# Optimization experiments

Hardware: AMD Instinct MI355X
Metric: run time of the kernel (lower is better)

The kernel has to match this reference:

```python
import jax, jax.numpy as jnp
import numpy as np

NEG_SLOPE = 0.2  # PyG GATConv default leaky_relu slope
N_NODES, N_EDGES, F_IN, HID = 25000, 200000, 64, 128


def gat_layer(x, src, dst, W, a_src, a_dst, b, heads, ch):
    """PyG-style GATConv (concat=True, eval mode). x:[N,Fin] -> [N,heads*ch]."""
    N = x.shape[0]
    h = (x @ W).reshape(N, heads, ch)                      # [N,H,C]
    al_s = jnp.sum(h * a_src, axis=-1)                     # [N,H]
    al_d = jnp.sum(h * a_dst, axis=-1)                     # [N,H]
    e = jax.nn.leaky_relu(al_s[src] + al_d[dst], NEG_SLOPE)  # [E,H]
    # segment softmax over incoming edges of each dst node (stable)
    e = e - jax.ops.segment_max(e, dst, num_segments=N)[dst]
    ex = jnp.exp(e)
    alpha = ex / jax.ops.segment_sum(ex, dst, num_segments=N)[dst]  # [E,H]
    out = jax.ops.segment_sum(h[src] * alpha[:, :, None], dst, num_segments=N)  # [N,H,C]
    return out.reshape(N, heads * ch) + b


def setup_inputs() -> dict:
    key = jax.random.key(0)
    ks = jax.random.split(key, 24)
    def g(k, shape, fan_in):
        return jax.random.normal(k, shape, dtype=jnp.float32) / np.sqrt(fan_in)
    inp = {
        "x": jax.random.normal(ks[0], (N_NODES, F_IN), dtype=jnp.float32),
        "edge_index": jax.random.randint(ks[1], (2, N_EDGES), 0, N_NODES, dtype=jnp.int64) if jax.config.jax_enable_x64 else jax.random.randint(ks[1], (2, N_EDGES), 0, N_NODES).astype(jnp.int32),
        "liquor_idx": jax.random.randint(ks[2], (4096,), 0, N_NODES),
        "ingredient_idx": jax.random.randint(ks[3], (4096,), 0, N_NODES),
        "W1": g(ks[4], (F_IN, 8 * HID), F_IN), "a_s1": g(ks[5], (8, HID), HID), "a_d1": g(ks[6], (8, HID), HID), "b1": jnp.zeros((8 * HID,), jnp.float32),
        "W2": g(ks[7], (8 * HID, 8 * HID), 8 * HID), "a_s2": g(ks[8], (8, HID), HID), "a_d2": g(ks[9], (8, HID), HID), "b2": jnp.zeros((8 * HID,), jnp.float32),
        "W3": g(ks[10], (8 * HID, HID), 8 * HID), "a_s3": g(ks[11], (1, HID), HID), "a_d3": g(ks[12], (1, HID), HID), "b3": jnp.zeros((HID,), jnp.float32),
        # MLP scorer: 256 -> 128 -> 64 -> 1
        "mw1": g(ks[13], (2 * HID, HID), 2 * HID), "mb1": jnp.zeros((HID,), jnp.float32),
        "mw2": g(ks[14], (HID, HID // 2), HID), "mb2": jnp.zeros((HID // 2,), jnp.float32),
        "mw3": g(ks[15], (HID // 2, 1), HID // 2), "mb3": jnp.zeros((1,), jnp.float32),
    }
    return inp


def reference(x, edge_index, liquor_idx, ingredient_idx,
              W1, a_s1, a_d1, b1, W2, a_s2, a_d2, b2, W3, a_s3, a_d3, b3,
              mw1, mb1, mw2, mb2, mw3, mb3):
    N = x.shape[0]
    loops = jnp.arange(N, dtype=edge_index.dtype)  # GATConv adds self-loops
    src = jnp.concatenate([edge_index[0], loops])
    dst = jnp.concatenate([edge_index[1], loops])
    h = jax.nn.relu(gat_layer(x, src, dst, W1, a_s1, a_d1, b1, 8, HID))
    h = jax.nn.relu(gat_layer(h, src, dst, W2, a_s2, a_d2, b2, 8, HID))
    h = gat_layer(h, src, dst, W3, a_s3, a_d3, b3, 1, HID)
    pair = jnp.concatenate([h[liquor_idx], h[ingredient_idx]], axis=-1)  # [B,256]
    z = jax.nn.relu(pair @ mw1 + mb1)
    z = jax.nn.relu(z @ mw2 + mb2)
    z = z @ mw3 + mb3
    return jax.nn.sigmoid(z).squeeze(-1)
```

## Files before the change

kernel.cpp:

```cpp
#include <hip/hip_runtime.h>
#include <math.h>

#define NEG_SLOPE 0.2f

typedef short short8 __attribute__((ext_vector_type(8)));
typedef float f32x4 __attribute__((ext_vector_type(4)));

__device__ __forceinline__ float lrelu(float x){ return x > 0.f ? x : NEG_SLOPE * x; }

__device__ __forceinline__ unsigned short f2bf(float f){
  union { float f; unsigned u; } v; v.f = f;
  unsigned r = v.u + 0x7fff + ((v.u >> 16) & 1);
  return (unsigned short)(r >> 16);
}
__device__ __forceinline__ float bf2f(unsigned short u){
  union { unsigned u; float f; } v; v.u = ((unsigned)u) << 16; return v.f;
}

__device__ __forceinline__ void gld16(const unsigned short* g, unsigned short* l){
  __builtin_amdgcn_global_load_lds(
      (const __attribute__((address_space(1))) unsigned int*)g,
      (__attribute__((address_space(3))) unsigned int*)l, 16, 0, 0);
}

__global__ void k_count(const int* __restrict__ dst, int* __restrict__ cnt, int E){
  int e = blockIdx.x*blockDim.x + threadIdx.x;
  if (e < E) atomicAdd(&cnt[dst[e]], 1);
}

__global__ void k_blockscan(const int* __restrict__ cnt, int* __restrict__ row,
                            int* __restrict__ aux, int n){
  __shared__ int buf[256];
  int t = threadIdx.x;
  int base = blockIdx.x * 256;
  int v = (base + t < n) ? cnt[base + t] : 0;
  buf[t] = v;
  __syncthreads();
  #pragma unroll
  for (int off = 1; off < 256; off <<= 1){
    int u = (t >= off) ? buf[t - off] : 0;
    __syncthreads();
    buf[t] += u;
    __syncthreads();
  }
  if (base + t < n) row[base + t + 1] = buf[t];
  if (t == 255) aux[blockIdx.x] = buf[255];
  if (blockIdx.x == 0 && t == 0) row[0] = 0;
}

__global__ void k_addoff(const int* __restrict__ aux, int* __restrict__ row, int n){
  __shared__ int s_pre;
  int b = blockIdx.x, t = threadIdx.x;
  if (t == 0){
    int pre = 0;
    for (int i = 0; i < b; ++i) pre += aux[i];
    s_pre = pre;
  }
  __syncthreads();
  int i = b * 256 + t;
  if (i < n) row[i + 1] += s_pre;
}

__global__ void k_scatter(const int* __restrict__ src, const int* __restrict__ dst,
                          const int* __restrict__ row, int* __restrict__ cur,
                          int* __restrict__ csr, int E){
  int e = blockIdx.x*blockDim.x + threadIdx.x;
  if (e < E){
    int d = dst[e];
    int p = atomicAdd(&cur[d], 1);
    csr[row[d] + p] = src[e];
  }
}

__global__ void k_prep(const float* __restrict__ x, unsigned short* __restrict__ xb, int nx, int nxb,
                       const float* __restrict__ W1, unsigned short* __restrict__ Wt1,
                       const float* __restrict__ W2, unsigned short* __restrict__ Wt2,
                       const float* __restrict__ W3, unsigned short* __restrict__ Wt3){
  __shared__ float tile[32][33];
  int b = blockIdx.x, t = threadIdx.x;
  if (b < nxb){
    int i0 = b * 2048 + t * 8;
    if (i0 + 8 <= nx){
      float4 f0 = *reinterpret_cast<const float4*>(x + i0);
      float4 f1 = *reinterpret_cast<const float4*>(x + i0 + 4);
      short8 o;
      o[0]=f2bf(f0.x); o[1]=f2bf(f0.y); o[2]=f2bf(f0.z); o[3]=f2bf(f0.w);
      o[4]=f2bf(f1.x); o[5]=f2bf(f1.y); o[6]=f2bf(f1.z); o[7]=f2bf(f1.w);
      *reinterpret_cast<short8*>(xb + i0) = o;
    } else {
      for (int k = 0; k < 8 && i0 + k < nx; ++k) xb[i0 + k] = f2bf(x[i0 + k]);
    }
    return;
  }
  const float* W; unsigned short* Wt; int K, N, ti;
  if (b < nxb + 64)            { W = W1; Wt = Wt1; K = 64;   N = 1024; ti = b - nxb;
                                 int kb = (ti & 1) * 32, nb = (ti >> 1) * 32;
                                 int tx = t & 31, ty = t >> 5;
                                 #pragma unroll
                                 for (int i = ty; i < 32; i += 8) tile[i][tx] = W[(size_t)(kb+i)*N + nb+tx];
                                 __syncthreads();
                                 #pragma unroll
                                 for (int i = ty; i < 32; i += 8) Wt[(size_t)(nb+i)*K + kb+tx] = f2bf(tile[tx][i]);
                                 return; }
  if (b < nxb + 64 + 1024)     { W = W2; Wt = Wt2; K = 1024; N = 1024; ti = b - nxb - 64; }
  else                         { W = W3; Wt = Wt3; K = 1024; N = 128;  ti = b - nxb - 64 - 1024; }
  int kb = (ti & 31) * 32, nb = (ti >> 5) * 32;
  int tx = t & 31, ty = t >> 5;
  #pragma unroll
  for (int i = ty; i < 32; i += 8) tile[i][tx] = W[(size_t)(kb+i)*N + nb+tx];
  __syncthreads();
  #pragma unroll
  for (int i = ty; i < 32; i += 8) Wt[(size_t)(nb+i)*K + kb+tx] = f2bf(tile[tx][i]);
}

template<int HEADS>
__global__ __launch_bounds__(256) void k_gemm_fused(
    const unsigned short* __restrict__ A,
    const unsigned short* __restrict__ Bt,
    unsigned short* __restrict__ C,
    const float* __restrict__ a_s, const float* __restrict__ a_d,
    float* __restrict__ ALS, float* __restrict__ ALD,
    int M, int N, int K, int gxc){
  __shared__ unsigned short SMEM[2 * 128 * 32];
  unsigned short* As = SMEM;
  unsigned short* Bs = SMEM + 128 * 32;
  const int nwg = gridDim.x;
  int bid = blockIdx.x;
  int swz = ((nwg & 7) == 0) ? ((bid & 7) * (nwg >> 3) + (bid >> 3)) : bid;
  const int bxi = swz % gxc, byi = swz / gxc;
  const int bm = byi * 128, bn = bxi * 128;
  const int head = bxi;
  const int tid  = threadIdx.x;
  const int lane = tid & 63, wave = tid >> 6;
  const int wr = wave >> 1, wc = wave & 1;
  const int lr = lane & 15, lk = lane >> 4;
  const int srow = wave * 16 + (lane >> 2);
  const int skc  = (lane & 3) * 8;
  int ar0 = bm + srow;      if (ar0 >= M) ar0 = M - 1;
  int ar1 = bm + srow + 64; if (ar1 >= M) ar1 = M - 1;
  const unsigned short* ga0 = A  + (size_t)ar0 * K + skc;
  const unsigned short* ga1 = A  + (size_t)ar1 * K + skc;
  const unsigned short* gb0 = Bt + (size_t)(bn + srow) * K + skc;
  const unsigned short* gb1 = Bt + (size_t)(bn + srow + 64) * K + skc;
  f32x4 acc[4][4] = {};
  for (int k0 = 0; k0 < K; k0 += 32){
    gld16(ga0 + k0, &As[(size_t)wave * 512]);
    gld16(ga1 + k0, &As[(size_t)(wave + 4) * 512]);
    gld16(gb0 + k0, &Bs[(size_t)wave * 512]);
    gld16(gb1 + k0, &Bs[(size_t)(wave + 4) * 512]);
    __syncthreads();
    short8 af[4], bg[4];
    #pragma unroll
    for (int m = 0; m < 4; ++m)
      af[m] = *reinterpret_cast<const short8*>(&As[(wr * 64 + m * 16 + lr) * 32 + lk * 8]);
    #pragma unroll
    for (int n = 0; n < 4; ++n)
      bg[n] = *reinterpret_cast<const short8*>(&Bs[(wc * 64 + n * 16 + lr) * 32 + lk * 8]);
    #pragma unroll
    for (int m = 0; m < 4; ++m)
      #pragma unroll
      for (int n = 0; n < 4; ++n)
        acc[m][n] = __builtin_amdgcn_mfma_f32_16x16x32_bf16(af[m], bg[n], acc[m][n], 0, 0, 0);
    __syncthreads();
  }
  #pragma unroll
  for (int m = 0; m < 4; ++m){
    #pragma unroll
    for (int j = 0; j < 4; ++j){
      int rowi = bm + wr * 64 + m * 16 + lk * 4 + j;
      if (rowi < M){
        #pragma unroll
        for (int n = 0; n < 4; ++n)
          C[(size_t)rowi * N + bn + wc * 64 + n * 16 + lr] = f2bf(acc[m][n][j]);
      }
    }
  }
  float as4[4], ad4[4];
  #pragma unroll
  for (int n = 0; n < 4; ++n){
    as4[n] = a_s[head * 128 + wc * 64 + n * 16 + lr];
    ad4[n] = a_d[head * 128 + wc * 64 + n * 16 + lr];
  }
  float* red = (float*)SMEM;
  #pragma unroll
  for (int m = 0; m < 4; ++m){
    #pragma unroll
    for (int j = 0; j < 4; ++j){
      float ps = 0.f;
      #pragma unroll
      for (int n = 0; n < 4; ++n) ps = fmaf(acc[m][n][j], as4[n], ps);
      red[(wr * 64 + m * 16 + lk * 4 + j) * 32 + wc * 16 + lr] = ps;
    }
  }
  __syncthreads();
  if (tid < 128){
    float s = 0.f;
    #pragma unroll
    for (int i = 0; i < 32; ++i) s += red[tid * 32 + ((i + tid) & 31)];
    int gr = bm + tid;
    if (gr < M) ALS[(size_t)gr * HEADS + head] = s;
  }
  __syncthreads();
  #pragma unroll
  for (int m = 0; m < 4; ++m){
    #pragma unroll
    for (int j = 0; j < 4; ++j){
      float pd = 0.f;
      #pragma unroll
      for (int n = 0; n < 4; ++n) pd = fmaf(acc[m][n][j], ad4[n], pd);
      red[(wr * 64 + m * 16 + lk * 4 + j) * 32 + wc * 16 + lr] = pd;
    }
  }
  __syncthreads();
  if (tid < 128){
    float s = 0.f;
    #pragma unroll
    for (int i = 0; i < 32; ++i) s += red[tid * 32 + ((i + tid) & 31)];
    int gr = bm + tid;
    if (gr < M) ALD[(size_t)gr * HEADS + head] = s;
  }
}

template<int HEADS, int VEC, int OUTBF>
__global__ void k_gat_bf(const unsigned short* __restrict__ hp, const float* __restrict__ al_s,
                         const float* __restrict__ al_d, const int* __restrict__ row,
                         const int* __restrict__ csr, const float* __restrict__ bias,
                         void* __restrict__ outv, int N, int do_relu){
  constexpr int TPH = 128 / VEC;
  int n = blockIdx.x;
  int t = threadIdx.x;
  int h = t / TPH;
  int c0 = (t % TPH) * VEC;
  float ald = al_d[(size_t)n * HEADS + h];
  float mA = lrelu(al_s[(size_t)n * HEADS + h] + ald);
  float lA = 1.f;
  float accA[VEC], accB[VEC];
  float mB = -1e30f, lB = 0.f;
  const unsigned short* hpn = hp + ((size_t)n * HEADS + h) * 128 + c0;
  if constexpr (VEC == 8){
    short8 hv8 = *reinterpret_cast<const short8*>(hpn);
    #pragma unroll
    for (int v = 0; v < 8; ++v){ accA[v] = bf2f((unsigned short)hv8[v]); accB[v] = 0.f; }
  } else {
    ushort2 hv2 = *reinterpret_cast<const ushort2*>(hpn);
    accA[0] = bf2f(hv2.x); accA[1] = bf2f(hv2.y);
    accB[0] = 0.f; accB[1] = 0.f;
  }
  int beg = row[n], end = row[n + 1];
  int j = beg;
  for (; j + 1 < end; j += 2){
    int s0 = csr[j], s1 = csr[j + 1];
    float e0 = lrelu(al_s[(size_t)s0 * HEADS + h] + ald);
    float e1 = lrelu(al_s[(size_t)s1 * HEADS + h] + ald);
    const unsigned short* p0 = hp + ((size_t)s0 * HEADS + h) * 128 + c0;
    const unsigned short* p1 = hp + ((size_t)s1 * HEADS + h) * 128 + c0;
    if constexpr (VEC == 8){
      short8 v0 = *reinterpret_cast<const short8*>(p0);
      short8 v1 = *reinterpret_cast<const short8*>(p1);
      float mn0 = fmaxf(mA, e0), mn1 = fmaxf(mB, e1);
      float sc0 = __expf(mA - mn0), sc1 = __expf(mB - mn1);
      float pw0 = __expf(e0 - mn0), pw1 = __expf(e1 - mn1);
      #pragma unroll
      for (int v = 0; v < 8; ++v){
        accA[v] = accA[v] * sc0 + pw0 * bf2f((unsigned short)v0[v]);
        accB[v] = accB[v] * sc1 + pw1 * bf2f((unsigned short)v1[v]);
      }
      lA = lA * sc0 + pw0; mA = mn0;
      lB = lB * sc1 + pw1; mB = mn1;
    } else {
      ushort2 v0 = *reinterpret_cast<const ushort2*>(p0);
      ushort2 v1 = *reinterpret_cast<const ushort2*>(p1);
      float mn0 = fmaxf(mA, e0), mn1 = fmaxf(mB, e1);
      float sc0 = __expf(mA - mn0), sc1 = __expf(mB - mn1);
      float pw0 = __expf(e0 - mn0), pw1 = __expf(e1 - mn1);
      accA[0] = accA[0] * sc0 + pw0 * bf2f(v0.x);
      accA[1] = accA[1] * sc0 + pw0 * bf2f(v0.y);
      accB[0] = accB[0] * sc1 + pw1 * bf2f(v1.x);
      accB[1] = accB[1] * sc1 + pw1 * bf2f(v1.y);
      lA = lA * sc0 + pw0; mA = mn0;
      lB = lB * sc1 + pw1; mB = mn1;
    }
  }
  if (j < end){
    int s0 = csr[j];
    float e0 = lrelu(al_s[(size_t)s0 * HEADS + h] + ald);
    const unsigned short* p0 = hp + ((size_t)s0 * HEADS + h) * 128 + c0;
    float mn0 = fmaxf(mA, e0);
    float sc0 = __expf(mA - mn0), pw0 = __expf(e0 - mn0);
    if constexpr (VEC == 8){
      short8 v0 = *reinterpret_cast<const short8*>(p0);
      #pragma unroll
      for (int v = 0; v < 8; ++v) accA[v] = accA[v] * sc0 + pw0 * bf2f((unsigned short)v0[v]);
    } else {
      ushort2 v0 = *reinterpret_cast<const ushort2*>(p0);
      accA[0] = accA[0] * sc0 + pw0 * bf2f(v0.x);
      accA[1] = accA[1] * sc0 + pw0 * bf2f(v0.y);
    }
    lA = lA * sc0 + pw0; mA = mn0;
  }
  float mn = fmaxf(mA, mB);
  float sA = __expf(mA - mn), sB = __expf(mB - mn);
  float l = lA * sA + lB * sB;
  float inv = 1.f / l;
  size_t ob = ((size_t)n * HEADS + h) * 128 + c0;
  #pragma unroll
  for (int v = 0; v < VEC; ++v){
    float o = (accA[v] * sA + accB[v] * sB) * inv + bias[h * 128 + c0 + v];
    if (do_relu) o = fmaxf(o, 0.f);
    if constexpr (OUTBF) ((unsigned short*)outv)[ob + v] = f2bf(o);
    else                 ((float*)outv)[ob + v] = o;
  }
}

__global__ void k_mlp(const float* __restrict__ h3, const int* __restrict__ liq,
                      const int* __restrict__ ing,
                      const float* __restrict__ mw1, const float* __restrict__ mb1,
                      const float* __restrict__ mw2, const float* __restrict__ mb2,
                      const float* __restrict__ mw3, const float* __restrict__ mb3,
                      float* __restrict__ out, int B){
  __shared__ float pairv[256];
  __shared__ float z1[128];
  __shared__ float z2[64];
  int r = blockIdx.x;
  int t = threadIdx.x;
  pairv[t]       = h3[(size_t)liq[r] * 128 + t];
  pairv[128 + t] = h3[(size_t)ing[r] * 128 + t];
  __syncthreads();
  float a1 = mb1[t];
  for (int k = 0; k < 256; ++k) a1 = fmaf(pairv[k], mw1[k * 128 + t], a1);
  z1[t] = fmaxf(a1, 0.f);
  __syncthreads();
  if (t < 64){
    float a2 = mb2[t];
    for (int k = 0; k < 128; ++k) a2 = fmaf(z1[k], mw2[k * 64 + t], a2);
    z2[t] = fmaxf(a2, 0.f);
  }
  __syncthreads();
  if (t < 64){
    float p = z2[t] * mw3[t];
    #pragma unroll
    for (int off = 32; off >= 1; off >>= 1) p += __shfl_xor(p, off);
    if (t == 0) out[r] = 1.f / (1.f + __expf(-(p + mb3[0])));
  }
}

extern "C" void kernel_launch(void* const* d_in, const int* in_sizes, int n_in,
                              void* d_out, int out_size, void* d_ws, size_t ws_size,
                              hipStream_t stream){
  const float* x   = (const float*)d_in[0];
  const int*   ei  = (const int*)  d_in[1];
  const int*   liq = (const int*)  d_in[2];
  const int*   ing = (const int*)  d_in[3];
  const float* W1  = (const float*)d_in[4];
  const float* as1 = (const float*)d_in[5];
  const float* ad1 = (const float*)d_in[6];
  const float* b1  = (const float*)d_in[7];
  const float* W2  = (const float*)d_in[8];
  const float* as2 = (const float*)d_in[9];
  const float* ad2 = (const float*)d_in[10];
  const float* b2  = (const float*)d_in[11];
  const float* W3  = (const float*)d_in[12];
  const float* as3 = (const float*)d_in[13];
  const float* ad3 = (const float*)d_in[14];
  const float* b3  = (const float*)d_in[15];
  const float* mw1 = (const float*)d_in[16];
  const float* mb1 = (const float*)d_in[17];
  const float* mw2 = (const float*)d_in[18];
  const float* mb2 = (const float*)d_in[19];
  const float* mw3 = (const float*)d_in[20];
  const float* mb3 = (const float*)d_in[21];
  float* out = (float*)d_out;

  const int N = in_sizes[0] / 64;
  const int E = in_sizes[1] / 2;
  const int B = in_sizes[2];
  const int* srcp = ei;
  const int* dstp = ei + E;

  char* w = (char*)d_ws;
  auto alloc = [&](size_t bytes) -> char* {
    char* p = w;
    w += (bytes + 255) & ~(size_t)255;
    return p;
  };
  unsigned short* P    = (unsigned short*)alloc((size_t)N * 1024 * 2);
  unsigned short* Hb   = (unsigned short*)alloc((size_t)N * 1024 * 2);
  float*          H3   = (float*)         alloc((size_t)N * 128 * 4);
  unsigned short* xb   = (unsigned short*)alloc((size_t)N * 64 * 2);
  unsigned short* Wt1  = (unsigned short*)alloc((size_t)1024 * 64 * 2);
  unsigned short* Wt2  = (unsigned short*)alloc((size_t)1024 * 1024 * 2);
  unsigned short* Wt3  = (unsigned short*)alloc((size_t)128 * 1024 * 2);
  float* ALS  = (float*)alloc((size_t)N * 8 * 4);
  float* ALD  = (float*)alloc((size_t)N * 8 * 4);
  int*   row  = (int*)  alloc((size_t)(N + 1) * 4);
  int*   cntcur = (int*)alloc((size_t)2 * N * 4);
  int*   cnt  = cntcur;
  int*   cur  = cntcur + N;
  int*   aux  = (int*)  alloc((size_t)256 * 4);
  int*   csr  = (int*)  alloc((size_t)E * 4);
  (void)ws_size; (void)n_in; (void)out_size;

  int nx = N * 64;
  int nxb = (nx + 2047) / 2048;
  k_prep<<<nxb + 64 + 1024 + 128, 256, 0, stream>>>(x, xb, nx, nxb, W1, Wt1, W2, Wt2, W3, Wt3);

  hipMemsetAsync(cntcur, 0, (size_t)2 * N * 4, stream);
  int eb = (E + 255) / 256;
  int nb = (N + 255) / 256;
  k_count<<<eb, 256, 0, stream>>>(dstp, cnt, E);
  k_blockscan<<<nb, 256, 0, stream>>>(cnt, row, aux, N);
  k_addoff<<<nb, 256, 0, stream>>>(aux, row, N);
  k_scatter<<<eb, 256, 0, stream>>>(srcp, dstp, row, cur, csr, E);

  const int mt = (N + 127) / 128;

  k_gemm_fused<8><<<8 * mt, 256, 0, stream>>>(xb, Wt1, P, as1, ad1, ALS, ALD, N, 1024, 64, 8);
  k_gat_bf<8,8,1><<<N, 128, 0, stream>>>(P, ALS, ALD, row, csr, b1, Hb, N, 1);

  k_gemm_fused<8><<<8 * mt, 256, 0, stream>>>(Hb, Wt2, P, as2, ad2, ALS, ALD, N, 1024, 1024, 8);
  k_gat_bf<8,8,1><<<N, 128, 0, stream>>>(P, ALS, ALD, row, csr, b2, Hb, N, 1);

  k_gemm_fused<1><<<1 * mt, 256, 0, stream>>>(Hb, Wt3, P, as3, ad3, ALS, ALD, N, 128, 1024, 1);
  k_gat_bf<1,2,0><<<N, 64, 0, stream>>>(P, ALS, ALD, row, csr, b3, H3, N, 0);

  k_mlp<<<B, 128, 0, stream>>>(H3, liq, ing, mw1, mb1, mw2, mb2, mw3, mb3, out, B);
}
```

Before: 363.3 us.

## Add 256x128-tile 8-wave GEMM with split-phase prefetch for layer-2 projection

Adds a new bf16 MFMA GEMM kernel for the 1024x1024 layer-2 projection. It uses 256-row tiles with 512 threads, double-buffered LDS filled by direct global-to-LDS loads, and B and A prefetches staggered across two MFMA phases with priority hints. It also computes both attention dot products (src and dst) in one shared-memory reduction pass. The larger tile is meant to raise operand reuse and overlap memory with compute. The cost is roughly 96KB of LDS per block and tight register use under launch_bounds(512,2), which can limit occupancy.

Result: no change. 356.7 us (-1.8%).

```diff
diff --git a/kernel.cpp b/kernel.cpp
--- a/kernel.cpp
+++ b/kernel.cpp
@@ -221,6 +221,160 @@
   }
 }
 
+__global__ __launch_bounds__(512, 2) void k_gemm256(
+    const unsigned short* __restrict__ A,
+    const unsigned short* __restrict__ Bt,
+    unsigned short* __restrict__ C,
+    const float* __restrict__ a_s, const float* __restrict__ a_d,
+    float* __restrict__ ALS, float* __restrict__ ALD,
+    int M, int N, int K, int gxc){
+  __shared__ unsigned short smem[2 * 24576];
+  const int nwg = gridDim.x;
+  int bid = blockIdx.x;
+  int swz = ((nwg & 7) == 0) ? ((bid & 7) * (nwg >> 3) + (bid >> 3)) : bid;
+  const int bxi = swz % gxc, byi = swz / gxc;
+  const int bm = byi * 256, bn = bxi * 128, head = bxi;
+  const int tid = threadIdx.x;
+  const int lane = tid & 63, wave = tid >> 6;
+  const int wr = wave >> 1, wc = wave & 1;
+  const int lr = lane & 15, lk = lane >> 4;
+  const int sr   = tid >> 3;
+  const int scol = ((tid & 7) << 3) ^ ((sr & 7) << 3);
+  size_t offA[4], offB[2];
+  #pragma unroll
+  for (int u = 0; u < 4; ++u){
+    int r = bm + u * 64 + sr; if (r >= M) r = M - 1;
+    offA[u] = (size_t)r * K + scol;
+  }
+  #pragma unroll
+  for (int u = 0; u < 2; ++u)
+    offB[u] = (size_t)(bn + u * 64 + sr) * K + scol;
+  const int wdst = (tid >> 6) * 512;
+
+  f32x4 acc[4][4] = {};
+  short8 af[4][2], bg[4][2];
+  const int NKT = K >> 6;
+  const int rsw = (lr & 7) << 3;
+
+  #pragma unroll
+  for (int u = 0; u < 4; ++u) gld16(A + offA[u], &smem[u * 4096 + wdst]);
+  #pragma unroll
+  for (int u = 0; u < 2; ++u) gld16(Bt + offB[u], &smem[16384 + u * 4096 + wdst]);
+  #pragma unroll
+  for (int u = 0; u < 4; ++u) gld16(A + offA[u] + 64, &smem[24576 + u * 4096 + wdst]);
+  asm volatile("s_waitcnt vmcnt(4)" ::: "memory");
+  __builtin_amdgcn_s_barrier();
+
+  for (int kt = 0; kt < NKT; ++kt){
+    const int s = kt & 1;
+    const unsigned short* sa = &smem[s * 24576];
+    const unsigned short* sb = &smem[s * 24576 + 16384];
+    #pragma unroll
+    for (int m = 0; m < 4; ++m){
+      int r = (wr * 64 + m * 16 + lr) * 64;
+      af[m][0] = *reinterpret_cast<const short8*>(&sa[r + ((lk * 8) ^ rsw)]);
+      af[m][1] = *reinterpret_cast<const short8*>(&sa[r + ((32 + lk * 8) ^ rsw)]);
+    }
+    #pragma unroll
+    for (int n = 0; n < 2; ++n){
+      int r = (wc * 64 + n * 16 + lr) * 64;
+      bg[n][0] = *reinterpret_cast<const short8*>(&sb[r + ((lk * 8) ^ rsw)]);
+      bg[n][1] = *reinterpret_cast<const short8*>(&sb[r + ((32 + lk * 8) ^ rsw)]);
+    }
+    if (kt + 1 < NKT){
+      int so = (s ^ 1) * 24576 + 16384;
+      gld16(Bt + offB[0] + (size_t)(kt + 1) * 64, &smem[so + wdst]);
+      gld16(Bt + offB[1] + (size_t)(kt + 1) * 64, &smem[so + 4096 + wdst]);
+    }
+    __builtin_amdgcn_s_barrier();
+    asm volatile("s_waitcnt lgkmcnt(0)" ::: "memory");
+    __builtin_amdgcn_sched_barrier(0);
+    __builtin_amdgcn_s_setprio(1);
+    #pragma unroll
+    for (int m = 0; m < 4; ++m)
+      #pragma unroll
+      for (int n = 0; n < 2; ++n){
+        acc[m][n] = __builtin_amdgcn_mfma_f32_16x16x32_bf16(af[m][0], bg[n][0], acc[m][n], 0, 0, 0);
+        acc[m][n] = __builtin_amdgcn_mfma_f32_16x16x32_bf16(af[m][1], bg[n][1], acc[m][n], 0, 0, 0);
+      }
+    __builtin_amdgcn_s_setprio(0);
+    __builtin_amdgcn_s_barrier();
+    #pragma unroll
+    for (int n = 2; n < 4; ++n){
+      int r = (wc * 64 + n * 16 + lr) * 64;
+      bg[n][0] = *reinterpret_cast<const short8*>(&sb[r + ((lk * 8) ^ rsw)]);
+      bg[n][1] = *reinterpret_cast<const short8*>(&sb[r + ((32 + lk * 8) ^ rsw)]);
+    }
+    if (kt + 2 < NKT){
+      int so = s * 24576;
+      #pragma unroll
+      for (int u = 0; u < 4; ++u)
+        gld16(A + offA[u] + (size_t)(kt + 2) * 64, &smem[so + u * 4096 + wdst]);
+    }
+    __builtin_amdgcn_s_barrier();
+    asm volatile("s_waitcnt lgkmcnt(0)" ::: "memory");
+    __builtin_amdgcn_sched_barrier(0);
+    __builtin_amdgcn_s_setprio(1);
+    #pragma unroll
+    for (int m = 0; m < 4; ++m)
+      #pragma unroll
+      for (int n = 2; n < 4; ++n){
+        acc[m][n] = __builtin_amdgcn_mfma_f32_16x16x32_bf16(af[m][0], bg[n][0], acc[m][n], 0, 0, 0);
+        acc[m][n] = __builtin_amdgcn_mfma_f32_16x16x32_bf16(af[m][1], bg[n][1], acc[m][n], 0, 0, 0);
+      }
+    __builtin_amdgcn_s_setprio(0);
+    asm volatile("s_waitcnt vmcnt(4)" ::: "memory");
+    __builtin_amdgcn_s_barrier();
+  }
+
+  #pragma unroll
+  for (int m = 0; m < 4; ++m)
+    #pragma unroll
+    for (int j = 0; j < 4; ++j){
+      int row = bm + wr * 64 + m * 16 + lk * 4 + j;
+      if (row < M){
+        #pragma unroll
+        for (int n = 0; n < 4; ++n)
+          C[(size_t)row * N + bn + wc * 64 + n * 16 + lr] = f2bf(acc[m][n][j]);
+      }
+    }
+  float as4[4], ad4[4];
+  #pragma unroll
+  for (int n = 0; n < 4; ++n){
+    as4[n] = a_s[head * 128 + wc * 64 + n * 16 + lr];
+    ad4[n] = a_d[head * 128 + wc * 64 + n * 16 + lr];
+  }
+  asm volatile("s_waitcnt vmcnt(0)" ::: "memory");
+  __builtin_amdgcn_s_barrier();
+  float2* red = (float2*)smem;
+  #pragma unroll
+  for (int m = 0; m < 4; ++m)
+    #pragma unroll
+    for (int j = 0; j < 4; ++j){
+      float ps = 0.f, pd = 0.f;
+      #pragma unroll
+      for (int n = 0; n < 4; ++n){
+        ps = fmaf(acc[m][n][j], as4[n], ps);
+        pd = fmaf(acc[m][n][j], ad4[n], pd);
+      }
+      red[(wr * 64 + m * 16 + lk * 4 + j) * 32 + wc * 16 + lr] = make_float2(ps, pd);
+    }
+  __syncthreads();
+  if (tid < 256){
+    float ss = 0.f, sd = 0.f;
+    #pragma unroll
+    for (int i = 0; i < 32; ++i){
+      float2 v = red[tid * 32 + ((i + tid) & 31)];
+      ss += v.x; sd += v.y;
+    }
+    int gr = bm + tid;
+    if (gr < M){
+      ALS[(size_t)gr * 8 + head] = ss;
+      ALD[(size_t)gr * 8 + head] = sd;
+    }
+  }
+}
+
 template<int HEADS, int VEC, int OUTBF>
 __global__ void k_gat_bf(const unsigned short* __restrict__ hp, const float* __restrict__ al_s,
                          const float* __restrict__ al_d, const int* __restrict__ row,
@@ -412,12 +566,13 @@
   k_addoff<<<nb, 256, 0, stream>>>(aux, row, N);
   k_scatter<<<eb, 256, 0, stream>>>(srcp, dstp, row, cur, csr, E);
 
-  const int mt = (N + 127) / 128;
+  const int mt  = (N + 127) / 128;
+  const int mt2 = (N + 255) / 256;
 
   k_gemm_fused<8><<<8 * mt, 256, 0, stream>>>(xb, Wt1, P, as1, ad1, ALS, ALD, N, 1024, 64, 8);
   k_gat_bf<8,8,1><<<N, 128, 0, stream>>>(P, ALS, ALD, row, csr, b1, Hb, N, 1);
 
-  k_gemm_fused<8><<<8 * mt, 256, 0, stream>>>(Hb, Wt2, P, as2, ad2, ALS, ALD, N, 1024, 1024, 8);
+  k_gemm256<<<8 * mt2, 512, 0, stream>>>(Hb, Wt2, P, as2, ad2, ALS, ALD, N, 1024, 1024, 8);
   k_gat_bf<8,8,1><<<N, 128, 0, stream>>>(P, ALS, ALD, row, csr, b2, Hb, N, 1);
 
   k_gemm_fused<1><<<1 * mt, 256, 0, stream>>>(Hb, Wt3, P, as3, ad3, ALS, ALD, N, 128, 1024, 1);
```
